# Optimization experiments

Measured on AMD Instinct MI355X. Metric: run time of the kernel, lower is better.

Reference implementation:

```python
import jax, jax.numpy as jnp
import numpy as np

T, B, IN, H, L = 512, 256, 64, 128, 5  # seq, batch, in_dim, hidden, layers


def _lstm_layer(x_seq, W_ih, W_hh, b_ih, b_hh):
    # x_seq: [T, B, D]; W_ih: [4H, D]; W_hh: [4H, H]; biases: [4H]
    # Precompute input contribution for all timesteps (big GEMM, compute-dense)
    pre = jnp.einsum('tbd,gd->tbg', x_seq, W_ih) + b_ih + b_hh  # [T, B, 4H]
    h0 = jnp.zeros((x_seq.shape[1], W_hh.shape[1]), x_seq.dtype)
    c0 = h0

    def step(carry, p):
        h, c = carry
        gates = p + h @ W_hh.T  # [B, 4H], PyTorch gate order i,f,g,o
        i, f, g, o = jnp.split(gates, 4, axis=-1)
        i = jax.nn.sigmoid(i)
        f = jax.nn.sigmoid(f)
        g = jnp.tanh(g)
        o = jax.nn.sigmoid(o)
        c = f * c + i * g
        h = o * jnp.tanh(c)
        return (h, c), h

    _, hs = jax.lax.scan(step, (h0, c0), pre)
    return hs  # [T, B, H]


def setup_inputs() -> dict:
    key = jax.random.key(0)
    ks = jax.random.split(key, 6)
    s = 1.0 / np.sqrt(H)  # PyTorch LSTM init scale
    return {
        'x': jax.random.normal(ks[0], (T, B, IN), jnp.float32),
        'W_ih0': jax.random.uniform(ks[1], (4 * H, IN), jnp.float32, -s, s),
        'W_ih_rest': jax.random.uniform(ks[2], (L - 1, 4 * H, H), jnp.float32, -s, s),
        'W_hh': jax.random.uniform(ks[3], (L, 4 * H, H), jnp.float32, -s, s),
        'b_ih': jax.random.uniform(ks[4], (L, 4 * H), jnp.float32, -s, s),
        'b_hh': jax.random.uniform(ks[5], (L, 4 * H), jnp.float32, -s, s),
    }


def reference(x, W_ih0, W_ih_rest, W_hh, b_ih, b_hh):
    # 5-layer stacked LSTM, eval mode (inter-layer dropout inactive).
    h = _lstm_layer(x, W_ih0, W_hh[0], b_ih[0], b_hh[0])
    for l in range(1, L):  # fixed small layer loop
        h = _lstm_layer(h, W_ih_rest[l - 1], W_hh[l], b_ih[l], b_hh[l])
    return h  # [T, B, H]
```

## Files before the change

kernel.cpp:

```cpp
#include <hip/hip_runtime.h>


typedef unsigned short ushort_t;
typedef unsigned int uint_t;
typedef unsigned long long ull_t;
typedef __attribute__((ext_vector_type(8))) short short8;
typedef __attribute__((ext_vector_type(4))) float floatx4;

#define T_STEPS 512
#define BATCH   256
#define HID     128
#define NL      5
#define NBG     16
#define RING_R  64
#define CHUNK   8
#define FLAG_STRIDE 16
#define SLOT_U  (BATCH * HID / 2)
#define RING_U  ((size_t)RING_R * SLOT_U)
#define WS_NEED (8192 + 4 * RING_U * 4)

__device__ __forceinline__ ushort_t f2bf(float f) {
  unsigned int u = __float_as_uint(f);
  u += 0x7FFF + ((u >> 16) & 1);
  return (ushort_t)(u >> 16);
}
__device__ __forceinline__ float sigm(float x) {
  float e = __builtin_amdgcn_exp2f(-1.442695041f * x);
  return __builtin_amdgcn_rcpf(1.0f + e);
}
__device__ __forceinline__ float tanh_(float x) {
  float e = __builtin_amdgcn_exp2f(-2.885390082f * x);
  float s = __builtin_amdgcn_rcpf(1.0f + e);
  return __builtin_fmaf(2.0f, s, -1.0f);
}
__device__ __forceinline__ int flag_ld(const int* p) {
  return __hip_atomic_load(p, __ATOMIC_RELAXED, __HIP_MEMORY_SCOPE_AGENT);
}

__global__ void init_flags(int* flags) {
  int i = blockIdx.x * 256 + threadIdx.x;
  if (i < NL * NBG * FLAG_STRIDE)
    __hip_atomic_store(&flags[i], 0, __ATOMIC_RELAXED,
                       __HIP_MEMORY_SCOPE_AGENT);
}

template <int KIN, bool SRC_F32, bool RING_OUT>
__device__ __forceinline__ void lstm_stage(
    const float* xf32,
    const uint_t* ring_in,
    const float* __restrict__ Wih, const float* __restrict__ Whh,
    const float* __restrict__ bih, const float* __restrict__ bhh,
    uint_t* ring_out,
    float* out_f32,
    int* up_flag, int* down_flag, int* my_flag, int bg)
{
  constexpr int KX = KIN / 32, KT = KX + 4;
  constexpr int AW = KIN + 128, AS = AW + 8;
  constexpr int NSTG = 16 * KIN / 4;

  const int tid  = threadIdx.x;
  const int wave = tid >> 6;
  const int lane = tid & 63;
  const int col  = lane & 15;
  const int quad = lane >> 4;
  const int j    = wave * 16 + col;

  __shared__ __align__(16) ushort_t Ah[2][16][AS];
  for (int i = tid; i < 2 * 16 * AS; i += 512) (&Ah[0][0][0])[i] = 0;

  short8 wf[4][KT];
#pragma unroll
  for (int nt = 0; nt < 4; ++nt) {
    int n = nt * 128 + j;
#pragma unroll
    for (int kt = 0; kt < KX; ++kt) {
      const float* p = Wih + n * KIN + kt * 32 + quad * 8;
      short8 w;
#pragma unroll
      for (int e = 0; e < 8; ++e) w[e] = (short)f2bf(p[e]);
      wf[nt][kt] = w;
    }
#pragma unroll
    for (int kt = 0; kt < 4; ++kt) {
      const float* p = Whh + n * 128 + kt * 32 + quad * 8;
      short8 w;
#pragma unroll
      for (int e = 0; e < 8; ++e) w[e] = (short)f2bf(p[e]);
      wf[nt][KX + kt] = w;
    }
  }
  const float bi  = bih[j]       + bhh[j];
  const float bf_ = bih[128 + j] + bhh[128 + j];
  const float bgi = bih[256 + j] + bhh[256 + j];
  const float bo  = bih[384 + j] + bhh[384 + j];

  floatx4 c = {0.f, 0.f, 0.f, 0.f};
  int down_seen = 0;
  int avail = 0;

  const int srow = tid / (KIN / 4), scol = (tid % (KIN / 4)) * 4;
  floatx4 xv = {0.f, 0.f, 0.f, 0.f};
  auto x_ld = [&](int t) {
    if constexpr (SRC_F32) {
      if (tid < NSTG && t < T_STEPS)
        xv = *(const floatx4*)(xf32 +
                               (size_t)(t * BATCH + bg * 16 + srow) * KIN + scol);
    }
  };
  auto x_st = [&](int t, ushort_t (*buf)[AS]) {
    if constexpr (SRC_F32) {
      if (tid < NSTG && t < T_STEPS) {
#pragma unroll
        for (int e = 0; e < 4; ++e) buf[srow][scol + e] = f2bf(xv[e]);
      }
    }
  };

  const int crow = tid >> 5;
  const int ccol = (tid & 31) * 4;
  ull_t pf = 0;
  auto r_ld = [&](int t) {
    if (t < T_STEPS)
      pf = __hip_atomic_load(
          (const ull_t*)(ring_in + (size_t)(t & (RING_R - 1)) * SLOT_U +
                         bg * 1024) + tid,
          __ATOMIC_RELAXED, __HIP_MEMORY_SCOPE_AGENT);
  };
  auto r_st = [&](int t, ushort_t (*buf)[AS]) {
    if (t < T_STEPS)
      *(ull_t*)(&buf[crow][ccol]) = pf;
  };

  __syncthreads();

  if constexpr (SRC_F32) {
    x_ld(0); x_st(0, Ah[0]); x_ld(1);
  } else {
    while ((avail = flag_ld(up_flag)) < 2) __builtin_amdgcn_s_sleep(1);
    asm volatile("" ::: "memory");
    r_ld(0); r_st(0, Ah[0]);
    r_ld(1);
  }
  __syncthreads();

  for (int t = 0; t < T_STEPS; ++t) {
    if ((t & (CHUNK - 1)) == 0 && t) {
      asm volatile("s_waitcnt vmcnt(0)\n\ts_barrier" ::: "memory");
      if (tid == 0)
        __hip_atomic_store(my_flag, t - 1, __ATOMIC_RELAXED,
                           __HIP_MEMORY_SCOPE_AGENT);
    }
    if constexpr (!SRC_F32) {
      if (t + 2 < T_STEPS && avail < t + 3) {
        while ((avail = flag_ld(up_flag)) < t + 3) __builtin_amdgcn_s_sleep(1);
      }
      asm volatile("" ::: "memory");
    }
    if constexpr (RING_OUT) {
      if (t > 0) {
        int s = t - 1;
        while (s - down_seen >= RING_R - 8) {
          down_seen = flag_ld(down_flag);
          if (s - down_seen >= RING_R - 8) __builtin_amdgcn_s_sleep(1);
        }
        asm volatile("" ::: "memory");
        ull_t hv8 = *(const ull_t*)(&Ah[t & 1][crow][KIN + ccol]);
        __hip_atomic_store(
            (ull_t*)(ring_out + (size_t)(s & (RING_R - 1)) * SLOT_U +
                     bg * 1024) + tid,
            hv8, __ATOMIC_RELAXED, __HIP_MEMORY_SCOPE_AGENT);
      }
    }

    ushort_t (*rd)[AS] = Ah[t & 1];
    ushort_t (*wr)[AS] = Ah[(t & 1) ^ 1];

    if constexpr (SRC_F32) { x_st(t + 1, wr); x_ld(t + 2); }
    else                   { r_st(t + 1, wr); r_ld(t + 2); }

    short8 af[KT];
#pragma unroll
    for (int kt = 0; kt < KT; ++kt)
      af[kt] = *(const short8*)(&rd[col][kt * 32 + quad * 8]);
    floatx4 a0 = {0, 0, 0, 0}, a1 = {0, 0, 0, 0}, a2 = {0, 0, 0, 0},
            a3 = {0, 0, 0, 0};
#pragma unroll
    for (int kt = 0; kt < KT; ++kt) {
      short8 a = af[kt];
      a0 = __builtin_amdgcn_mfma_f32_16x16x32_bf16(a, wf[0][kt], a0, 0, 0, 0);
      a1 = __builtin_amdgcn_mfma_f32_16x16x32_bf16(a, wf[1][kt], a1, 0, 0, 0);
      a2 = __builtin_amdgcn_mfma_f32_16x16x32_bf16(a, wf[2][kt], a2, 0, 0, 0);
      a3 = __builtin_amdgcn_mfma_f32_16x16x32_bf16(a, wf[3][kt], a3, 0, 0, 0);
    }

#pragma unroll
    for (int r = 0; r < 4; ++r) {
      float iv = sigm(a0[r] + bi);
      float fv = sigm(a1[r] + bf_);
      float gv = tanh_(a2[r] + bgi);
      float ov = sigm(a3[r] + bo);
      float cn = __builtin_fmaf(fv, c[r], iv * gv);
      c[r] = cn;
      float hv = ov * tanh_(cn);
      wr[quad * 4 + r][KIN + j] = f2bf(hv);
      if constexpr (!RING_OUT) {
        out_f32[((size_t)t * BATCH + bg * 16 + quad * 4 + r) * HID + j] = hv;
      }
    }

    asm volatile("s_waitcnt lgkmcnt(0)\n\ts_barrier" ::: "memory");
  }

  if constexpr (RING_OUT) {
    int s = T_STEPS - 1;
    while (s - down_seen >= RING_R - 8) {
      down_seen = flag_ld(down_flag);
      if (s - down_seen >= RING_R - 8) __builtin_amdgcn_s_sleep(1);
    }
    asm volatile("" ::: "memory");
    ull_t hv8 = *(const ull_t*)(&Ah[T_STEPS & 1][crow][KIN + ccol]);
    __hip_atomic_store(
        (ull_t*)(ring_out + (size_t)(s & (RING_R - 1)) * SLOT_U + bg * 1024) +
            tid,
        hv8, __ATOMIC_RELAXED, __HIP_MEMORY_SCOPE_AGENT);
  }
  asm volatile("s_waitcnt vmcnt(0)\n\ts_barrier" ::: "memory");
  if (tid == 0)
    __hip_atomic_store(my_flag, T_STEPS, __ATOMIC_RELAXED,
                       __HIP_MEMORY_SCOPE_AGENT);
}

__global__ __launch_bounds__(512) void lstm_pipe(
    const float* x, const float* Wih0, const float* WihR,
    const float* Whh, const float* bih, const float* bhh,
    float* out, uint_t* ring, int* flags)
{
  const int l  = blockIdx.x >> 4;
  const int bg = blockIdx.x & 15;
  int* mine = flags + (l * NBG + bg) * FLAG_STRIDE;
  int* up   = (l > 0) ? flags + ((l - 1) * NBG + bg) * FLAG_STRIDE : nullptr;
  int* down = (l < 4) ? flags + ((l + 1) * NBG + bg) * FLAG_STRIDE : nullptr;

  if (l == 0) {
    lstm_stage<64, true, true>(x, nullptr, Wih0, Whh, bih, bhh,
                               ring, nullptr, up, down, mine, bg);
  } else if (l < 4) {
    lstm_stage<128, false, true>(nullptr, ring + (size_t)(l - 1) * RING_U,
                                 WihR + (size_t)(l - 1) * 512 * 128,
                                 Whh + (size_t)l * 512 * 128,
                                 bih + l * 512, bhh + l * 512,
                                 ring + (size_t)l * RING_U, nullptr,
                                 up, down, mine, bg);
  } else {
    lstm_stage<128, false, false>(nullptr, ring + (size_t)3 * RING_U,
                                  WihR + (size_t)3 * 512 * 128,
                                  Whh + (size_t)4 * 512 * 128,
                                  bih + 4 * 512, bhh + 4 * 512,
                                  nullptr, out, up, nullptr, mine, bg);
  }
}

template <int KIN>
__global__ __launch_bounds__(512) void lstm_layer(
    const float* xin, float* hout,
    const float* __restrict__ Wih, const float* __restrict__ Whh,
    const float* __restrict__ bih, const float* __restrict__ bhh)
{
  constexpr int KX = KIN / 32, KT = KX + 4;
  constexpr int AW = KIN + 128, AS = AW + 8;
  constexpr int NSTG = 16 * KIN / 4;

  const int bg = blockIdx.x, tid = threadIdx.x;
  const int wave = tid >> 6, lane = tid & 63;
  const int col = lane & 15, quad = lane >> 4;
  const int j = wave * 16 + col;

  __shared__ __align__(16) ushort_t Ah[2][16][AS];
  for (int i = tid; i < 2 * 16 * AS; i += 512) (&Ah[0][0][0])[i] = 0;

  short8 wf[4][KT];
#pragma unroll
  for (int nt = 0; nt < 4; ++nt) {
    int n = nt * 128 + j;
#pragma unroll
    for (int kt = 0; kt < KX; ++kt) {
      const float* p = Wih + n * KIN + kt * 32 + quad * 8;
      short8 w;
#pragma unroll
      for (int e = 0; e < 8; ++e) w[e] = (short)f2bf(p[e]);
      wf[nt][kt] = w;
    }
#pragma unroll
    for (int kt = 0; kt < 4; ++kt) {
      const float* p = Whh + n * 128 + kt * 32 + quad * 8;
      short8 w;
#pragma unroll
      for (int e = 0; e < 8; ++e) w[e] = (short)f2bf(p[e]);
      wf[nt][KX + kt] = w;
    }
  }
  const float bi  = bih[j]       + bhh[j];
  const float bf_ = bih[128 + j] + bhh[128 + j];
  const float bgi = bih[256 + j] + bhh[256 + j];
  const float bo  = bih[384 + j] + bhh[384 + j];

  floatx4 c = {0.f, 0.f, 0.f, 0.f};
  const int srow = tid / (KIN / 4), scol = (tid % (KIN / 4)) * 4;
  floatx4 xv = {0.f, 0.f, 0.f, 0.f};
  auto stage_load = [&](int t) {
    if (tid < NSTG && t < T_STEPS)
      xv = *(const floatx4*)(xin + (size_t)(t * BATCH + bg * 16 + srow) * KIN + scol);
  };
  auto stage_store = [&](int t, ushort_t (*buf)[AS]) {
    if (tid < NSTG && t < T_STEPS) {
#pragma unroll
      for (int e = 0; e < 4; ++e) buf[srow][scol + e] = f2bf(xv[e]);
    }
  };
  __syncthreads();
  stage_load(0); stage_store(0, Ah[0]); stage_load(1);
  __syncthreads();

  for (int t = 0; t < T_STEPS; ++t) {
    ushort_t (*rd)[AS] = Ah[t & 1];
    ushort_t (*wr)[AS] = Ah[(t & 1) ^ 1];
    short8 af[KT];
#pragma unroll
    for (int kt = 0; kt < KT; ++kt)
      af[kt] = *(const short8*)(&rd[col][kt * 32 + quad * 8]);
    floatx4 a0 = {0, 0, 0, 0}, a1 = {0, 0, 0, 0}, a2 = {0, 0, 0, 0},
            a3 = {0, 0, 0, 0};
#pragma unroll
    for (int kt = 0; kt < KT; ++kt) {
      short8 a = af[kt];
      a0 = __builtin_amdgcn_mfma_f32_16x16x32_bf16(a, wf[0][kt], a0, 0, 0, 0);
      a1 = __builtin_amdgcn_mfma_f32_16x16x32_bf16(a, wf[1][kt], a1, 0, 0, 0);
      a2 = __builtin_amdgcn_mfma_f32_16x16x32_bf16(a, wf[2][kt], a2, 0, 0, 0);
      a3 = __builtin_amdgcn_mfma_f32_16x16x32_bf16(a, wf[3][kt], a3, 0, 0, 0);
    }
    stage_store(t + 1, wr);
    stage_load(t + 2);
    size_t obase = (size_t)(t * BATCH + bg * 16) * HID + j;
#pragma unroll
    for (int r = 0; r < 4; ++r) {
      int row = quad * 4 + r;
      float iv = sigm(a0[r] + bi);
      float fv = sigm(a1[r] + bf_);
      float gv = tanh_(a2[r] + bgi);
      float ov = sigm(a3[r] + bo);
      float cn = __builtin_fmaf(fv, c[r], iv * gv);
      c[r] = cn;
      float hv = ov * tanh_(cn);
      wr[row][KIN + j] = f2bf(hv);
      hout[obase + (size_t)row * HID] = hv;
    }
    __syncthreads();
  }
}

extern "C" void kernel_launch(void* const* d_in, const int* in_sizes, int n_in,
                              void* d_out, int out_size, void* d_ws,
                              size_t ws_size, hipStream_t stream) {
  const float* x    = (const float*)d_in[0];
  const float* Wih0 = (const float*)d_in[1];
  const float* WihR = (const float*)d_in[2];
  const float* Whh  = (const float*)d_in[3];
  const float* bih  = (const float*)d_in[4];
  const float* bhh  = (const float*)d_in[5];
  float* out = (float*)d_out;

  if (ws_size >= WS_NEED) {
    int* flags = (int*)d_ws;
    uint_t* ring = (uint_t*)((char*)d_ws + 8192);
    init_flags<<<(NL * NBG * FLAG_STRIDE + 255) / 256, 256, 0, stream>>>(flags);
    lstm_pipe<<<NL * NBG, 512, 0, stream>>>(x, Wih0, WihR, Whh, bih, bhh,
                                            out, ring, flags);
  } else {
    lstm_layer<64><<<16, 512, 0, stream>>>(x, out, Wih0, Whh, bih, bhh);
    for (int l = 1; l < 5; ++l)
      lstm_layer<128><<<16, 512, 0, stream>>>(
          out, out, WihR + (size_t)(l - 1) * 512 * 128,
          Whh + (size_t)l * 512 * 128, bih + l * 512, bhh + l * 512);
  }
}
```

Before: 945.1 us.

## Prefetch layer inputs into an 8-deep LDS ring with polled flag mirrors

Splits the LDS activation buffer into an 8-slot input ring and a double-buffered hidden-state buffer. Each layer block can now prefetch up to seven timesteps of upstream input ahead of use instead of two. Upstream and downstream progress flags are polled once per step by thread 0 and mirrored into LDS, which takes global flag loads off the critical path for most threads. Flag publishing moves from every 8 steps to every 4, and the downstream start waits for 18 ready steps. This adds LDS use, more bookkeeping and a more intricate ordering between the flag protocol and the ring contents.

```diff
diff --git a/kernel.cpp b/kernel.cpp
--- a/kernel.cpp
+++ b/kernel.cpp
@@ -6,6 +6,7 @@
 typedef unsigned long long ull_t;
 typedef __attribute__((ext_vector_type(8))) short short8;
 typedef __attribute__((ext_vector_type(4))) float floatx4;
+typedef __attribute__((ext_vector_type(2))) float floatx2;
 
 #define T_STEPS 512
 #define BATCH   256
@@ -13,11 +14,12 @@
 #define NL      5
 #define NBG     16
 #define RING_R  64
-#define CHUNK   8
+#define PRIME   18
 #define FLAG_STRIDE 16
 #define SLOT_U  (BATCH * HID / 2)
 #define RING_U  ((size_t)RING_R * SLOT_U)
 #define WS_NEED (8192 + 4 * RING_U * 4)
+#define LDS_BYTES 43552
 
 __device__ __forceinline__ ushort_t f2bf(float f) {
   unsigned int u = __float_as_uint(f);
@@ -35,6 +37,14 @@
 }
 __device__ __forceinline__ int flag_ld(const int* p) {
   return __hip_atomic_load(p, __ATOMIC_RELAXED, __HIP_MEMORY_SCOPE_AGENT);
+}
+__device__ __forceinline__ ull_t ring_ld8(const uint_t* base, int tid) {
+  return __hip_atomic_load((const ull_t*)base + tid, __ATOMIC_RELAXED,
+                           __HIP_MEMORY_SCOPE_AGENT);
+}
+__device__ __forceinline__ void ring_st8(uint_t* base, int tid, ull_t v) {
+  __hip_atomic_store((ull_t*)base + tid, v, __ATOMIC_RELAXED,
+                     __HIP_MEMORY_SCOPE_AGENT);
 }
 
 __global__ void init_flags(int* flags) {
@@ -46,6 +56,7 @@
 
 template <int KIN, bool SRC_F32, bool RING_OUT>
 __device__ __forceinline__ void lstm_stage(
+    unsigned char* lds,
     const float* xf32,
     const uint_t* ring_in,
     const float* __restrict__ Wih, const float* __restrict__ Whh,
@@ -55,8 +66,15 @@
     int* up_flag, int* down_flag, int* my_flag, int bg)
 {
   constexpr int KX = KIN / 32, KT = KX + 4;
-  constexpr int AW = KIN + 128, AS = AW + 8;
-  constexpr int NSTG = 16 * KIN / 4;
+  constexpr int XS = KIN + 8;
+  constexpr int HS = 128 + 8;
+
+  typedef ushort_t (*XT)[16][XS];
+  typedef ushort_t (*HT)[16][HS];
+  XT Xr = (XT)lds;
+  HT Hr = (HT)(lds + (size_t)8 * 16 * XS * 2);
+  int* upm = (int*)(lds + (size_t)8 * 16 * XS * 2 + (size_t)2 * 16 * HS * 2);
+  int* dnm = upm + 4;
 
   const int tid  = threadIdx.x;
   const int wave = tid >> 6;
@@ -64,9 +82,14 @@
   const int col  = lane & 15;
   const int quad = lane >> 4;
   const int j    = wave * 16 + col;
-
-  __shared__ __align__(16) ushort_t Ah[2][16][AS];
-  for (int i = tid; i < 2 * 16 * AS; i += 512) (&Ah[0][0][0])[i] = 0;
+  const int frow = tid >> 5;
+  const int fc   = tid & 31;
+
+  for (int i = tid; i < 2 * 16 * HS; i += 512) (&Hr[0][0][0])[i] = 0;
+  if (tid == 0) {
+#pragma unroll
+    for (int i = 0; i < 4; ++i) { upm[i] = 0; dnm[i] = 0; }
+  }
 
   short8 wf[4][KT];
 #pragma unroll
@@ -95,93 +118,101 @@
   const float bo  = bih[384 + j] + bhh[384 + j];
 
   floatx4 c = {0.f, 0.f, 0.f, 0.f};
-  int down_seen = 0;
-  int avail = 0;
-
-  const int srow = tid / (KIN / 4), scol = (tid % (KIN / 4)) * 4;
-  floatx4 xv = {0.f, 0.f, 0.f, 0.f};
-  auto x_ld = [&](int t) {
-    if constexpr (SRC_F32) {
-      if (tid < NSTG && t < T_STEPS)
-        xv = *(const floatx4*)(xf32 +
-                               (size_t)(t * BATCH + bg * 16 + srow) * KIN + scol);
-    }
-  };
-  auto x_st = [&](int t, ushort_t (*buf)[AS]) {
-    if constexpr (SRC_F32) {
-      if (tid < NSTG && t < T_STEPS) {
-#pragma unroll
-        for (int e = 0; e < 4; ++e) buf[srow][scol + e] = f2bf(xv[e]);
-      }
-    }
-  };
-
-  const int crow = tid >> 5;
-  const int ccol = (tid & 31) * 4;
+  int nf;
+  int pu = 0, pd = 0;
   ull_t pf = 0;
-  auto r_ld = [&](int t) {
-    if (t < T_STEPS)
-      pf = __hip_atomic_load(
-          (const ull_t*)(ring_in + (size_t)(t & (RING_R - 1)) * SLOT_U +
-                         bg * 1024) + tid,
-          __ATOMIC_RELAXED, __HIP_MEMORY_SCOPE_AGENT);
-  };
-  auto r_st = [&](int t, ushort_t (*buf)[AS]) {
-    if (t < T_STEPS)
-      *(ull_t*)(&buf[crow][ccol]) = pf;
-  };
+  floatx2 pxf = {0.f, 0.f};
 
   __syncthreads();
 
-  if constexpr (SRC_F32) {
-    x_ld(0); x_st(0, Ah[0]); x_ld(1);
+  if constexpr (!SRC_F32) {
+    int v = 0;
+    while ((v = flag_ld(up_flag)) < PRIME) __builtin_amdgcn_s_sleep(1);
+    asm volatile("" ::: "memory");
+    if (tid == 0) {
+#pragma unroll
+      for (int i = 0; i < 4; ++i) upm[i] = v;
+      pu = v;
+    }
+    ull_t pr[8];
+#pragma unroll
+    for (int s = 0; s < 8; ++s)
+      pr[s] = ring_ld8(ring_in + (size_t)s * SLOT_U + bg * 1024, tid);
+#pragma unroll
+    for (int s = 0; s < 8; ++s)
+      *(ull_t*)(&Xr[s][frow][fc * 4]) = pr[s];
   } else {
-    while ((avail = flag_ld(up_flag)) < 2) __builtin_amdgcn_s_sleep(1);
-    asm volatile("" ::: "memory");
-    r_ld(0); r_st(0, Ah[0]);
-    r_ld(1);
-  }
-  __syncthreads();
+    floatx2 pr[8];
+#pragma unroll
+    for (int s = 0; s < 8; ++s)
+      pr[s] = *(const floatx2*)(xf32 +
+                                ((size_t)s * BATCH + bg * 16 + frow) * 64 +
+                                fc * 2);
+#pragma unroll
+    for (int s = 0; s < 8; ++s)
+      *(uint_t*)(&Xr[s][frow][fc * 2]) =
+          (uint_t)f2bf(pr[s][0]) | ((uint_t)f2bf(pr[s][1]) << 16);
+  }
+  nf = 8;
+  asm volatile("s_waitcnt lgkmcnt(0)\n\ts_barrier" ::: "memory");
 
   for (int t = 0; t < T_STEPS; ++t) {
-    if ((t & (CHUNK - 1)) == 0 && t) {
+    if ((t & 3) == 0 && t >= 4) {
       asm volatile("s_waitcnt vmcnt(0)\n\ts_barrier" ::: "memory");
       if (tid == 0)
         __hip_atomic_store(my_flag, t - 1, __ATOMIC_RELAXED,
                            __HIP_MEMORY_SCOPE_AGENT);
     }
+    const int am = upm[t & 3];
+    const int dn = dnm[t & 3];
+
     if constexpr (!SRC_F32) {
-      if (t + 2 < T_STEPS && avail < t + 3) {
-        while ((avail = flag_ld(up_flag)) < t + 3) __builtin_amdgcn_s_sleep(1);
+      if (nf == t) {
+        while (flag_ld(up_flag) < t + 1) __builtin_amdgcn_s_sleep(1);
+        asm volatile("" ::: "memory");
+        ull_t e = ring_ld8(
+            ring_in + (size_t)(t & (RING_R - 1)) * SLOT_U + bg * 1024, tid);
+        *(ull_t*)(&Xr[t & 7][frow][fc * 4]) = e;
+        nf = t + 1;
+        asm volatile("s_waitcnt lgkmcnt(0)\n\ts_barrier" ::: "memory");
       }
-      asm volatile("" ::: "memory");
-    }
+    }
+
     if constexpr (RING_OUT) {
-      if (t > 0) {
-        int s = t - 1;
-        while (s - down_seen >= RING_R - 8) {
-          down_seen = flag_ld(down_flag);
-          if (s - down_seen >= RING_R - 8) __builtin_amdgcn_s_sleep(1);
+      if (t >= 1) {
+        const int s = t - 1;
+        if (s - dn > RING_R - 16) {
+          while (s - flag_ld(down_flag) > RING_R - 16)
+            __builtin_amdgcn_s_sleep(1);
+          asm volatile("" ::: "memory");
         }
-        asm volatile("" ::: "memory");
-        ull_t hv8 = *(const ull_t*)(&Ah[t & 1][crow][KIN + ccol]);
-        __hip_atomic_store(
-            (ull_t*)(ring_out + (size_t)(s & (RING_R - 1)) * SLOT_U +
-                     bg * 1024) + tid,
-            hv8, __ATOMIC_RELAXED, __HIP_MEMORY_SCOPE_AGENT);
+        ull_t h8 = *(const ull_t*)(&Hr[t & 1][frow][fc * 4]);
+        ring_st8(ring_out + (size_t)(s & (RING_R - 1)) * SLOT_U + bg * 1024,
+                 tid, h8);
       }
     }
 
-    ushort_t (*rd)[AS] = Ah[t & 1];
-    ushort_t (*wr)[AS] = Ah[(t & 1) ^ 1];
-
-    if constexpr (SRC_F32) { x_st(t + 1, wr); x_ld(t + 2); }
-    else                   { r_st(t + 1, wr); r_ld(t + 2); }
+    bool dofetch;
+    if constexpr (SRC_F32) {
+      dofetch = (nf <= t + 7) && (nf < T_STEPS);
+      if (dofetch)
+        pxf = *(const floatx2*)(xf32 +
+                                ((size_t)nf * BATCH + bg * 16 + frow) * 64 +
+                                fc * 2);
+    } else {
+      dofetch = (nf <= t + 7) && (nf < T_STEPS) && (am >= nf + 1);
+      if (dofetch)
+        pf = ring_ld8(
+            ring_in + (size_t)(nf & (RING_R - 1)) * SLOT_U + bg * 1024, tid);
+    }
 
     short8 af[KT];
 #pragma unroll
-    for (int kt = 0; kt < KT; ++kt)
-      af[kt] = *(const short8*)(&rd[col][kt * 32 + quad * 8]);
+    for (int kt = 0; kt < KX; ++kt)
+      af[kt] = *(const short8*)(&Xr[t & 7][col][kt * 32 + quad * 8]);
+#pragma unroll
+    for (int kt = 0; kt < 4; ++kt)
+      af[KX + kt] = *(const short8*)(&Hr[t & 1][col][kt * 32 + quad * 8]);
     floatx4 a0 = {0, 0, 0, 0}, a1 = {0, 0, 0, 0}, a2 = {0, 0, 0, 0},
             a3 = {0, 0, 0, 0};
 #pragma unroll
@@ -193,6 +224,18 @@
       a3 = __builtin_amdgcn_mfma_f32_16x16x32_bf16(a, wf[3][kt], a3, 0, 0, 0);
     }
 
+    if (tid == 0) {
+      if constexpr (!SRC_F32) {
+        upm[(t + 2) & 3] = pu;
+        pu = flag_ld(up_flag);
+      }
+      if constexpr (RING_OUT) {
+        dnm[(t + 2) & 3] = pd;
+        pd = flag_ld(down_flag);
+      }
+    }
+
+    ushort_t (*wr)[HS] = Hr[(t & 1) ^ 1];
 #pragma unroll
     for (int r = 0; r < 4; ++r) {
       float iv = sigm(a0[r] + bi);
@@ -202,27 +245,31 @@
       float cn = __builtin_fmaf(fv, c[r], iv * gv);
       c[r] = cn;
       float hv = ov * tanh_(cn);
-      wr[quad * 4 + r][KIN + j] = f2bf(hv);
+      wr[quad * 4 + r][j] = f2bf(hv);
       if constexpr (!RING_OUT) {
         out_f32[((size_t)t * BATCH + bg * 16 + quad * 4 + r) * HID + j] = hv;
       }
     }
 
+    if (dofetch) {
+      if constexpr (SRC_F32)
+        *(uint_t*)(&Xr[nf & 7][frow][fc * 2]) =
+            (uint_t)f2bf(pxf[0]) | ((uint_t)f2bf(pxf[1]) << 16);
+      else
+        *(ull_t*)(&Xr[nf & 7][frow][fc * 4]) = pf;
+      ++nf;
+    }
+
     asm volatile("s_waitcnt lgkmcnt(0)\n\ts_barrier" ::: "memory");
   }
 
   if constexpr (RING_OUT) {
-    int s = T_STEPS - 1;
-    while (s - down_seen >= RING_R - 8) {
-      down_seen = flag_ld(down_flag);
-      if (s - down_seen >= RING_R - 8) __builtin_amdgcn_s_sleep(1);
-    }
+    const int s = T_STEPS - 1;
+    while (s - flag_ld(down_flag) > RING_R - 16) __builtin_amdgcn_s_sleep(1);
     asm volatile("" ::: "memory");
-    ull_t hv8 = *(const ull_t*)(&Ah[T_STEPS & 1][crow][KIN + ccol]);
-    __hip_atomic_store(
-        (ull_t*)(ring_out + (size_t)(s & (RING_R - 1)) * SLOT_U + bg * 1024) +
-            tid,
-        hv8, __ATOMIC_RELAXED, __HIP_MEMORY_SCOPE_AGENT);
+    ull_t h8 = *(const ull_t*)(&Hr[T_STEPS & 1][frow][fc * 4]);
+    ring_st8(ring_out + (size_t)(s & (RING_R - 1)) * SLOT_U + bg * 1024, tid,
+             h8);
   }
   asm volatile("s_waitcnt vmcnt(0)\n\ts_barrier" ::: "memory");
   if (tid == 0)
@@ -235,6 +282,7 @@
     const float* Whh, const float* bih, const float* bhh,
     float* out, uint_t* ring, int* flags)
 {
+  __shared__ __align__(16) unsigned char lds_raw[LDS_BYTES];
   const int l  = blockIdx.x >> 4;
   const int bg = blockIdx.x & 15;
   int* mine = flags + (l * NBG + bg) * FLAG_STRIDE;
@@ -242,17 +290,19 @@
   int* down = (l < 4) ? flags + ((l + 1) * NBG + bg) * FLAG_STRIDE : nullptr;
 
   if (l == 0) {
-    lstm_stage<64, true, true>(x, nullptr, Wih0, Whh, bih, bhh,
+    lstm_stage<64, true, true>(lds_raw, x, nullptr, Wih0, Whh, bih, bhh,
                                ring, nullptr, up, down, mine, bg);
   } else if (l < 4) {
-    lstm_stage<128, false, true>(nullptr, ring + (size_t)(l - 1) * RING_U,
+    lstm_stage<128, false, true>(lds_raw, nullptr,
+                                 ring + (size_t)(l - 1) * RING_U,
                                  WihR + (size_t)(l - 1) * 512 * 128,
                                  Whh + (size_t)l * 512 * 128,
                                  bih + l * 512, bhh + l * 512,
                                  ring + (size_t)l * RING_U, nullptr,
                                  up, down, mine, bg);
   } else {
-    lstm_stage<128, false, false>(nullptr, ring + (size_t)3 * RING_U,
+    lstm_stage<128, false, false>(lds_raw, nullptr,
+                                  ring + (size_t)3 * RING_U,
                                   WihR + (size_t)3 * 512 * 128,
                                   Whh + (size_t)4 * 512 * 128,
                                   bih + 4 * 512, bhh + 4 * 512,
```

After: 888.4 us. -6.0%, faster.
